# Performance work log

Measured on AMD Instinct MI355X. Metric: run time of the kernel, lower is better.

## Reference

```python
import jax, jax.numpy as jnp
import numpy as np

B = 1024
N_CPGS = 20000
N_FREQS = N_CPGS // 2 + 1  # 10001
HIDDEN = (256, 128, 64)
LN_EPS = 1e-5


def setup_inputs() -> dict:
    key = jax.random.key(0)
    keys = jax.random.split(key, 16)
    inp = {"x": jax.random.normal(keys[0], (B, N_CPGS), dtype=jnp.float32)}
    in_dim = N_FREQS
    for i, h in enumerate(HIDDEN):
        inp[f"W{i}"] = jax.random.normal(keys[1 + i], (h, in_dim), dtype=jnp.float32) * 0.01
        inp[f"alpha{i}"] = jnp.full((h, in_dim), 0.01, dtype=jnp.float32)
        inp[f"b{i}"] = jnp.zeros((h,), dtype=jnp.float32)
        inp[f"eta{i}"] = jnp.asarray(0.1, dtype=jnp.float32)
        inp[f"g{i}"] = jnp.ones((h,), dtype=jnp.float32)   # LayerNorm gamma
        inp[f"be{i}"] = jnp.zeros((h,), dtype=jnp.float32)  # LayerNorm beta
        in_dim = h
    inp["head_w"] = jax.random.normal(keys[10], (1, in_dim), dtype=jnp.float32) * (1.0 / np.sqrt(in_dim))
    inp["head_b"] = jnp.zeros((1,), dtype=jnp.float32)
    return inp


def _hebbian_layer(x, W, alpha, b, eta):
    # y_slow = x W^T + b;  plastic[b,i] = eta * tanh(y_slow)[b,i] * sum_j sigmoid(alpha)[i,j] * x_norm[b,j] * x[b,j]
    y_slow = jnp.einsum('bd,hd->bh', x, W) + b
    x_norm = x / (jnp.linalg.norm(x, axis=-1, keepdims=True) + 1e-8)
    c = x_norm * x  # (B, in) -- collapses the (B,out,in) outer-product trace algebraically
    plastic = eta * jnp.tanh(y_slow) * jnp.einsum('bd,hd->bh', c, jax.nn.sigmoid(alpha))
    return y_slow + plastic


def _layer_norm(h, g, be):
    mu = jnp.mean(h, axis=-1, keepdims=True)
    var = jnp.mean((h - mu) ** 2, axis=-1, keepdims=True)
    return (h - mu) * jax.lax.rsqrt(var + LN_EPS) * g + be


def reference(x, W0, alpha0, b0, eta0, g0, be0,
              W1, alpha1, b1, eta1, g1, be1,
              W2, alpha2, b2, eta2, g2, be2,
              head_w, head_b):
    # FFT spectral front-end
    xc = x - jnp.mean(x, axis=1, keepdims=True)
    h = jnp.log1p(jnp.abs(jnp.fft.rfft(xc, axis=1)))  # (B, N_FREQS)
    params = [(W0, alpha0, b0, eta0, g0, be0),
              (W1, alpha1, b1, eta1, g1, be1),
              (W2, alpha2, b2, eta2, g2, be2)]
    for (W, a, b, eta, g, be) in params:
        h = jax.nn.gelu(_layer_norm(_hebbian_layer(h, W, a, b, eta), g, be), approximate=False)
        # dropout is identity in eval mode
    return (jnp.einsum('bd,od->bo', h, head_w) + head_b)[:, 0]  # (B,)
```

## Files before the change

kernel.cpp:

```cpp
#include <hip/hip_runtime.h>
#include <hip/hip_bf16.h>
#include <math.h>

typedef short bf16x8 __attribute__((ext_vector_type(8)));
typedef float f32x4 __attribute__((ext_vector_type(4)));

static __device__ __forceinline__ unsigned short f2bf(float f) {
    unsigned int u = __float_as_uint(f);
    unsigned int r = (u + 0x7fffu + ((u >> 16) & 1u)) >> 16;
    return (unsigned short)r;
}

static __device__ __forceinline__ bf16x8 sq_bf16x8(bf16x8 a) {
    bf16x8 r;
    #pragma unroll
    for (int i = 0; i < 8; ++i) {
        unsigned int u = ((unsigned int)(unsigned short)a[i]) << 16;
        float f = __uint_as_float(u);
        f *= f;
        r[i] = (short)f2bf(f);
    }
    return r;
}

static __device__ __forceinline__ float gelu_f(float x) {
    return 0.5f * x * (1.f + erff(x * 0.70710678118654752f));
}

static __device__ __forceinline__ void gload_lds16(const void* g, void* l) {
    __builtin_amdgcn_global_load_lds(
        (const __attribute__((address_space(1))) unsigned int*)g,
        (__attribute__((address_space(3))) unsigned int*)l, 16, 0, 0);
}

static __device__ __forceinline__ int ldsmap(int i) { return i + (i >> 6); }

static __device__ __forceinline__ int rev4(int k) {
    int d0 = k % 10; k /= 10;
    int d1 = k % 10; k /= 10;
    int d2 = k % 10; int d3 = k / 10;
    return d0 * 1000 + d1 * 100 + d2 * 10 + d3;
}

__global__ __launch_bounds__(256)
void init_tables_kernel(unsigned int* __restrict__ idxTab)
{
    int i = blockIdx.x * 256 + threadIdx.x;
    if (i < 10001) {
        int k1 = (i == 10000) ? 0 : i;
        int k2 = (k1 == 0) ? 0 : 10000 - k1;
        unsigned a = (unsigned)ldsmap(rev4(k1));
        unsigned b = (unsigned)ldsmap(rev4(k2));
        idxTab[i] = a | (b << 16);
    }
}

static __device__ __forceinline__ void dft5(
    float a0r, float a0i, float a1r, float a1i, float a2r, float a2i,
    float a3r, float a3i, float a4r, float a4i,
    float* Xr, float* Xi)
{
    const float c1 = 0.30901699437494742f, c2 = -0.80901699437494745f;
    const float s1 = 0.95105651629515357f, s2 = 0.58778525229247312f;
    float t1r = a1r + a4r, t1i = a1i + a4i;
    float d1r = a1r - a4r, d1i = a1i - a4i;
    float t2r = a2r + a3r, t2i = a2i + a3i;
    float d2r = a2r - a3r, d2i = a2i - a3i;
    Xr[0] = a0r + t1r + t2r; Xi[0] = a0i + t1i + t2i;
    float m1r = a0r + c1 * t1r + c2 * t2r, m1i = a0i + c1 * t1i + c2 * t2i;
    float m2r = a0r + c2 * t1r + c1 * t2r, m2i = a0i + c2 * t1i + c1 * t2i;
    float n1r = s1 * d1r + s2 * d2r, n1i = s1 * d1i + s2 * d2i;
    float n2r = s2 * d1r - s1 * d2r, n2i = s2 * d1i - s1 * d2i;
    Xr[1] = m1r + n1i; Xi[1] = m1i - n1r;
    Xr[4] = m1r - n1i; Xi[4] = m1i + n1r;
    Xr[2] = m2r + n2i; Xi[2] = m2i - n2r;
    Xr[3] = m2r - n2i; Xi[3] = m2i + n2r;
}

template<int S>
static __device__ __forceinline__ void radix10_core(
    float* __restrict__ reb, float* __restrict__ imb,
    const float* ar, const float* ai, int base, int j)
{
    constexpr int L  = (S == 0) ? 1000 : (S == 1) ? 100 : (S == 2) ? 10 : 1;
    constexpr int SC = (S == 0) ? 1 : (S == 1) ? 10 : (S == 2) ? 100 : 1000;
    constexpr bool TW = (S != 3);

    const float WR[5] = {1.f, 0.80901699437494745f, 0.30901699437494742f,
                         -0.30901699437494742f, -0.80901699437494745f};
    const float WI[5] = {0.f, -0.58778525229247312f, -0.95105651629515357f,
                         -0.95105651629515357f, -0.58778525229247312f};

    float Er[5], Ei[5], Or[5], Oi[5];
    dft5(ar[0], ai[0], ar[2], ai[2], ar[4], ai[4], ar[6], ai[6], ar[8], ai[8], Er, Ei);
    dft5(ar[1], ai[1], ar[3], ai[3], ar[5], ai[5], ar[7], ai[7], ar[9], ai[9], Or, Oi);
    #pragma unroll
    for (int k = 1; k < 5; ++k) {
        float tr = Or[k] * WR[k] - Oi[k] * WI[k];
        Oi[k] = Or[k] * WI[k] + Oi[k] * WR[k];
        Or[k] = tr;
    }

    if (TW) {
        const float ang = (float)(j * SC) * -6.28318530717958648e-4f;
        float w1c, w1s;
        __sincosf(ang, &w1s, &w1c);
        float twr[10], twi[10];
        twr[0] = 1.f; twi[0] = 0.f;
        #pragma unroll
        for (int t = 1; t < 10; ++t) {
            twr[t] = twr[t - 1] * w1c - twi[t - 1] * w1s;
            twi[t] = twr[t - 1] * w1s + twi[t - 1] * w1c;
        }
        #pragma unroll
        for (int k = 0; k < 5; ++k) {
            float xr0 = Er[k] + Or[k], xi0 = Ei[k] + Oi[k];
            float xr1 = Er[k] - Or[k], xi1 = Ei[k] - Oi[k];
            int i0 = ldsmap(base + k * L);
            int i1 = ldsmap(base + (k + 5) * L);
            if (k == 0) {
                reb[i0] = xr0;
                imb[i0] = xi0;
            } else {
                reb[i0] = xr0 * twr[k] - xi0 * twi[k];
                imb[i0] = xr0 * twi[k] + xi0 * twr[k];
            }
            reb[i1] = xr1 * twr[k + 5] - xi1 * twi[k + 5];
            imb[i1] = xr1 * twi[k + 5] + xi1 * twr[k + 5];
        }
    } else {
        #pragma unroll
        for (int k = 0; k < 5; ++k) {
            int i0 = ldsmap(base + k * L);
            int i1 = ldsmap(base + (k + 5) * L);
            reb[i0] = Er[k] + Or[k]; imb[i0] = Ei[k] + Oi[k];
            reb[i1] = Er[k] - Or[k]; imb[i1] = Ei[k] - Oi[k];
        }
    }
}

template<int S>
static __device__ __forceinline__ void radix10_stage(
    float* __restrict__ reb, float* __restrict__ imb, int tid)
{
    constexpr int L = (S == 1) ? 100 : (S == 2) ? 10 : 1;
    for (int w = tid; w < 1000; w += 512) {
        int g, j;
        if (S == 3) { g = w; j = 0; }
        else        { g = w / L; j = w - g * L; }
        const int base = g * (10 * L) + j;
        float ar[10], ai[10];
        #pragma unroll
        for (int u = 0; u < 10; ++u) {
            int idx = ldsmap(base + u * L);
            ar[u] = reb[idx];
            ai[u] = imb[idx];
        }
        radix10_core<S>(reb, imb, ar, ai, base, j);
    }
}

__global__ __launch_bounds__(512, 4)
void fft_prep_kernel(const float* __restrict__ x,
                     unsigned short* __restrict__ hb,
                     float* __restrict__ hnorm,
                     const float* __restrict__ W0, const float* __restrict__ A0,
                     unsigned short* __restrict__ Wb, unsigned short* __restrict__ Sb,
                     const float* __restrict__ W1, const float* __restrict__ A1,
                     const float* __restrict__ W2, const float* __restrict__ A2,
                     float* __restrict__ W1T, float* __restrict__ S1T,
                     float* __restrict__ W2T, float* __restrict__ S2T,
                     const unsigned int* __restrict__ idxTab)
{
    if (blockIdx.x >= 1024) {
        int idx = (blockIdx.x - 1024) * 512 + threadIdx.x;
        if (idx < 1280128) {
            const bool isW = idx < 640064;
            const int f4 = isW ? idx : idx - 640064;
            const float* src = isW ? W0 : A0;
            unsigned short* dst = isW ? Wb : Sb;
            float4 v = ((const float4*)src)[f4];
            float e[4] = {v.x, v.y, v.z, v.w};
            int flat = f4 * 4;
            int row = flat / 10001;
            int col = flat - row * 10001;
            #pragma unroll
            for (int i = 0; i < 4; ++i) {
                if (col == 10001) { row++; col = 0; }
                float val = isW ? e[i] : 1.f / (1.f + expf(-e[i]));
                dst[(size_t)row * 10240 + col] = f2bf(val);
                col++;
            }
        } else if (idx < 1341312) {
            int i = idx - 1280128;
            int row = i / 239;
            int col = 10001 + (i - row * 239);
            Wb[(size_t)row * 10240 + col] = 0;
            Sb[(size_t)row * 10240 + col] = 0;
        } else if (idx < 1423232) {
            int o = idx - 1341312;
            if (o < 32768) {
                int d = o >> 7, h = o & 127;
                W1T[o] = W1[h * 256 + d];
            } else if (o < 65536) {
                int p = o - 32768;
                int d = p >> 7, h = p & 127;
                S1T[p] = 1.f / (1.f + expf(-A1[h * 256 + d]));
            } else if (o < 73728) {
                int p = o - 65536;
                int d = p >> 6, h = p & 63;
                W2T[p] = W2[h * 128 + d];
            } else {
                int p = o - 73728;
                int d = p >> 6, h = p & 63;
                S2T[p] = 1.f / (1.f + expf(-A2[h * 128 + d]));
            }
        }
        return;
    }

    __shared__ float reb[10156];
    __shared__ float imb[10156];
    __shared__ float redbuf[8];

    const int b = blockIdx.x;
    const int tid = threadIdx.x;
    const int lane = tid & 63;
    const int wv = tid >> 6;

    const float2* z2 = (const float2*)(x + (size_t)b * 20000);
    for (int w = tid; w < 1000; w += 512) {
        float ar[10], ai[10];
        #pragma unroll
        for (int u = 0; u < 10; ++u) {
            float2 v = z2[w + u * 1000];
            ar[u] = v.x; ai[u] = v.y;
        }
        radix10_core<0>(reb, imb, ar, ai, w, w);
    }
    __syncthreads();
    radix10_stage<1>(reb, imb, tid);
    __syncthreads();
    radix10_stage<2>(reb, imb, tid);
    __syncthreads();
    radix10_stage<3>(reb, imb, tid);
    __syncthreads();

    float ct, st;
    __sincosf((float)tid * -3.14159265358979324e-4f, &st, &ct);
    const float RC = 0.987091579f;
    const float RS = -0.160156842f;
    float sumsq = 0.f;
    unsigned short* hrow = hb + (size_t)b * 10240;
    #pragma unroll
    for (int i = 0; i < 20; ++i) {
        int k = tid + i * 512;
        float hval = 0.f;
        if (k > 0 && k <= 10000) {
            unsigned pp = idxTab[k];
            int i1 = (int)(pp & 0xffffu);
            int i2 = (int)(pp >> 16);
            float zr = reb[i1], zi = imb[i1];
            float wr = reb[i2], wi = imb[i2];
            float er = 0.5f * (zr + wr);
            float ei = 0.5f * (zi - wi);
            float odr = 0.5f * (zi + wi);
            float odi = -0.5f * (zr - wr);
            float xre = er + ct * odr - st * odi;
            float xim = ei + ct * odi + st * odr;
            hval = __logf(1.f + sqrtf(xre * xre + xim * xim));
        }
        hrow[k] = f2bf(hval);
        sumsq += hval * hval;
        float nct = ct * RC - st * RS;
        st = ct * RS + st * RC;
        ct = nct;
    }
    #pragma unroll
    for (int o = 32; o; o >>= 1) sumsq += __shfl_xor(sumsq, o);
    __syncthreads();
    if (lane == 0) redbuf[wv] = sumsq;
    __syncthreads();
    if (tid == 0) {
        float tsq = 0.f;
        #pragma unroll
        for (int i = 0; i < 8; ++i) tsq += redbuf[i];
        hnorm[b] = 1.f / (sqrtf(tsq) + 1e-8f);
    }
}

__global__ __launch_bounds__(256, 3)
void gemm0_kernel(const unsigned short* __restrict__ hb,
                  const unsigned short* __restrict__ Wb, const unsigned short* __restrict__ Sb,
                  float* __restrict__ Py, float* __restrict__ Pp)
{
    __shared__ unsigned short Ah[128 * 64];
    __shared__ unsigned short Bw[64 * 64];
    __shared__ unsigned short Bs[64 * 64];

    const int t = threadIdx.x;
    const int lin = blockIdx.x;
    const int xcd = lin & 7;
    const int sub = lin >> 3;
    const int z = xcd * 2 + (sub & 1);
    const int tile = sub >> 1;
    const int b0 = (tile & 7) * 128;
    const int n0 = (tile >> 3) * 64;

    const int lane = t & 63;
    const int wv = t >> 6;
    const int ml = lane & 15;
    const int q4 = lane >> 4;
    const int s0 = q4 ^ (ml & 7);

    const int sub8 = lane >> 3;
    const int sl = lane & 7;
    const int gsw = sl ^ sub8;

    f32x4 accY[2][4], accP[2][4];
    #pragma unroll
    for (int mt = 0; mt < 2; ++mt)
        #pragma unroll
        for (int nt = 0; nt < 4; ++nt) {
            accY[mt][nt] = (f32x4){0.f, 0.f, 0.f, 0.f};
            accP[mt][nt] = (f32x4){0.f, 0.f, 0.f, 0.f};
        }

    const int kbase = z * 640;

    for (int step = 0; step < 10; ++step) {
        const int k0 = kbase + step * 64;
        __syncthreads();
        #pragma unroll
        for (int j = 0; j < 4; ++j) {
            const int c = wv * 4 + j;
            const size_t go = (size_t)(b0 + c * 8 + sub8) * 10240 + k0 + gsw * 8;
            gload_lds16(&hb[go], &Ah[c * 512]);
        }
        #pragma unroll
        for (int j = 0; j < 2; ++j) {
            const int c = wv * 2 + j;
            const size_t go = (size_t)(n0 + c * 8 + sub8) * 10240 + k0 + gsw * 8;
            gload_lds16(&Wb[go], &Bw[c * 512]);
            gload_lds16(&Sb[go], &Bs[c * 512]);
        }
        __syncthreads();

        #pragma unroll
        for (int kk = 0; kk < 2; ++kk) {
            const int slot = (s0 ^ (kk << 2)) << 3;
            bf16x8 ah[2], ac[2], bw[4], bs[4];
            #pragma unroll
            for (int mt = 0; mt < 2; ++mt) {
                int mrow = wv * 32 + mt * 16 + ml;
                ah[mt] = *(const bf16x8*)&Ah[mrow * 64 + slot];
                ac[mt] = sq_bf16x8(ah[mt]);
            }
            #pragma unroll
            for (int nt = 0; nt < 4; ++nt) {
                int nrow = nt * 16 + ml;
                bw[nt] = *(const bf16x8*)&Bw[nrow * 64 + slot];
                bs[nt] = *(const bf16x8*)&Bs[nrow * 64 + slot];
            }
            #pragma unroll
            for (int mt = 0; mt < 2; ++mt)
                #pragma unroll
                for (int nt = 0; nt < 4; ++nt) {
                    accY[mt][nt] = __builtin_amdgcn_mfma_f32_16x16x32_bf16(ah[mt], bw[nt], accY[mt][nt], 0, 0, 0);
                    accP[mt][nt] = __builtin_amdgcn_mfma_f32_16x16x32_bf16(ac[mt], bs[nt], accP[mt][nt], 0, 0, 0);
                }
        }
    }

    const int rq = q4 * 4;
    #pragma unroll
    for (int mt = 0; mt < 2; ++mt)
        #pragma unroll
        for (int nt = 0; nt < 4; ++nt)
            #pragma unroll
            for (int r = 0; r < 4; ++r) {
                int m = b0 + wv * 32 + mt * 16 + rq + r;
                int n = n0 + nt * 16 + ml;
                size_t o = ((size_t)z * 1024 + m) * 256 + n;
                Py[o] = accY[mt][nt][r];
                Pp[o] = accP[mt][nt][r];
            }
}

__global__ __launch_bounds__(256)
void combine_tail_kernel(const float* __restrict__ Py, const float* __restrict__ Pp,
                 const float* __restrict__ hnorm,
                 const float* __restrict__ b0v, const float* __restrict__ eta0p,
                 const float* __restrict__ g0, const float* __restrict__ be0,
                 const float* __restrict__ W1T, const float* __restrict__ S1T,
                 const float* __restrict__ b1, const float* __restrict__ eta1p,
                 const float* __restrict__ g1, const float* __restrict__ be1,
                 const float* __restrict__ W2T, const float* __restrict__ S2T,
                 const float* __restrict__ b2, const float* __restrict__ eta2p,
                 const float* __restrict__ g2, const float* __restrict__ be2,
                 const float* __restrict__ hw, const float* __restrict__ hbod,
                 float* __restrict__ out)
{
    __shared__ float sh[2][256];
    __shared__ float sc[2][256];
    __shared__ float sv[2][128];
    __shared__ float sh2[2][128];
    __shared__ float sc2[2][128];
    __shared__ float sv2[2][64];
    __shared__ float p2a[2][2][64];
    __shared__ float p2b[2][2][64];
    __shared__ float redA[4][2];
    __shared__ float redB[4][2];

    const int t = threadIdx.x;
    const int b0 = blockIdx.x * 2;
    const int lane = t & 63;
    const int wv = t >> 6;

    const float e0 = eta0p[0];
    const float bias0 = b0v[t];
    float ys[2] = {0.f, 0.f}, ps[2] = {0.f, 0.f};
    #pragma unroll 4
    for (int s = 0; s < 16; ++s)
        #pragma unroll
        for (int r = 0; r < 2; ++r) {
            size_t o = ((size_t)s * 1024 + b0 + r) * 256 + t;
            ys[r] += Py[o];
            ps[r] += Pp[o];
        }
    float v[2];
    #pragma unroll
    for (int r = 0; r < 2; ++r) {
        float p = ps[r] * hnorm[b0 + r];
        float y = ys[r] + bias0;
        v[r] = y + e0 * tanhf(y) * p;
    }

    float s1[2], s2[2];
    #pragma unroll
    for (int r = 0; r < 2; ++r) { s1[r] = v[r]; s2[r] = v[r] * v[r]; }
    #pragma unroll
    for (int o = 32; o; o >>= 1)
        #pragma unroll
        for (int r = 0; r < 2; ++r) { s1[r] += __shfl_xor(s1[r], o); s2[r] += __shfl_xor(s2[r], o); }
    if (lane == 0)
        #pragma unroll
        for (int r = 0; r < 2; ++r) { redA[wv][r] = s1[r]; redB[wv][r] = s2[r]; }
    __syncthreads();

    const float gg = g0[t], bb = be0[t];
    float gl[2], s3[2];
    #pragma unroll
    for (int r = 0; r < 2; ++r) {
        float sum = redA[0][r] + redA[1][r] + redA[2][r] + redA[3][r];
        float sumsq = redB[0][r] + redB[1][r] + redB[2][r] + redB[3][r];
        float mu = sum * (1.f / 256.f);
        float var = sumsq * (1.f / 256.f) - mu * mu;
        float u = (v[r] - mu) * rsqrtf(var + 1e-5f) * gg + bb;
        gl[r] = gelu_f(u);
        s3[r] = gl[r] * gl[r];
    }
    #pragma unroll
    for (int o = 32; o; o >>= 1)
        #pragma unroll
        for (int r = 0; r < 2; ++r) s3[r] += __shfl_xor(s3[r], o);
    __syncthreads();
    if (lane == 0)
        #pragma unroll
        for (int r = 0; r < 2; ++r) redA[wv][r] = s3[r];
    __syncthreads();
    #pragma unroll
    for (int r = 0; r < 2; ++r) {
        float gsq = redA[0][r] + redA[1][r] + redA[2][r] + redA[3][r];
        float inv = 1.f / (sqrtf(gsq) + 1e-8f);
        sh[r][t] = gl[r];
        sc[r][t] = gl[r] * gl[r] * inv;
    }
    __syncthreads();

    const int hcol = t & 127;
    const int r1 = t >> 7;
    float ya = 0.f, pa = 0.f;
    #pragma unroll 8
    for (int d = 0; d < 256; ++d) {
        ya += sh[r1][d] * W1T[d * 128 + hcol];
        pa += sc[r1][d] * S1T[d * 128 + hcol];
    }
    {
        const float e1 = eta1p[0];
        float y = ya + b1[hcol];
        sv[r1][hcol] = y + e1 * tanhf(y) * pa;
    }
    __syncthreads();

    if (wv < 2) {
        int r = wv;
        float v0 = sv[r][lane];
        float v1 = sv[r][lane + 64];
        float s = v0 + v1, sq = v0 * v0 + v1 * v1;
        #pragma unroll
        for (int o = 32; o; o >>= 1) { s += __shfl_xor(s, o); sq += __shfl_xor(sq, o); }
        float mu = s * (1.f / 128.f);
        float var = sq * (1.f / 128.f) - mu * mu;
        float rs = rsqrtf(var + 1e-5f);
        float u0 = (v0 - mu) * rs * g1[lane] + be1[lane];
        float u1 = (v1 - mu) * rs * g1[lane + 64] + be1[lane + 64];
        float ge0 = gelu_f(u0);
        float ge1 = gelu_f(u1);
        float gsq = ge0 * ge0 + ge1 * ge1;
        #pragma unroll
        for (int o = 32; o; o >>= 1) gsq += __shfl_xor(gsq, o);
        float inv = 1.f / (sqrtf(gsq) + 1e-8f);
        sh2[r][lane] = ge0; sh2[r][lane + 64] = ge1;
        sc2[r][lane] = ge0 * ge0 * inv; sc2[r][lane + 64] = ge1 * ge1 * inv;
    }
    __syncthreads();

    {
        const int h2c = t & 63;
        const int r = (t >> 6) & 1;
        const int dh = t >> 7;
        float yb = 0.f, pb = 0.f;
        #pragma unroll 8
        for (int dd = 0; dd < 64; ++dd) {
            int d = dh * 64 + dd;
            yb += sh2[r][d] * W2T[d * 64 + h2c];
            pb += sc2[r][d] * S2T[d * 64 + h2c];
        }
        p2a[dh][r][h2c] = yb;
        p2b[dh][r][h2c] = pb;
    }
    __syncthreads();
    if (t < 128) {
        const int h2c = t & 63;
        const int r = t >> 6;
        const float e2 = eta2p[0];
        float yb = p2a[0][r][h2c] + p2a[1][r][h2c];
        float pb = p2b[0][r][h2c] + p2b[1][r][h2c];
        float y = yb + b2[h2c];
        sv2[r][h2c] = y + e2 * tanhf(y) * pb;
    }
    __syncthreads();

    if (wv < 2) {
        int r = wv;
        float v0 = sv2[r][lane];
        float s = v0, sq = v0 * v0;
        #pragma unroll
        for (int o = 32; o; o >>= 1) { s += __shfl_xor(s, o); sq += __shfl_xor(sq, o); }
        float mu = s * (1.f / 64.f);
        float var = sq * (1.f / 64.f) - mu * mu;
        float rs = rsqrtf(var + 1e-5f);
        float u = (v0 - mu) * rs * g2[lane] + be2[lane];
        float g = gelu_f(u);
        float hc = g * hw[lane];
        #pragma unroll
        for (int o = 32; o; o >>= 1) hc += __shfl_xor(hc, o);
        if (lane == 0) out[b0 + r] = hc + hbod[0];
    }
}

extern "C" void kernel_launch(void* const* d_in, const int* in_sizes, int n_in,
                              void* d_out, int out_size, void* d_ws, size_t ws_size,
                              hipStream_t stream)
{
    const float* x    = (const float*)d_in[0];
    const float* W0   = (const float*)d_in[1];
    const float* A0   = (const float*)d_in[2];
    const float* b0   = (const float*)d_in[3];
    const float* eta0 = (const float*)d_in[4];
    const float* g0   = (const float*)d_in[5];
    const float* be0  = (const float*)d_in[6];
    const float* W1   = (const float*)d_in[7];
    const float* A1   = (const float*)d_in[8];
    const float* b1   = (const float*)d_in[9];
    const float* eta1 = (const float*)d_in[10];
    const float* g1   = (const float*)d_in[11];
    const float* be1  = (const float*)d_in[12];
    const float* W2   = (const float*)d_in[13];
    const float* A2   = (const float*)d_in[14];
    const float* b2   = (const float*)d_in[15];
    const float* eta2 = (const float*)d_in[16];
    const float* g2   = (const float*)d_in[17];
    const float* be2  = (const float*)d_in[18];
    const float* hw   = (const float*)d_in[19];
    const float* hbod = (const float*)d_in[20];
    float* out = (float*)d_out;

    char* w = (char*)d_ws;
    unsigned short* hb  = (unsigned short*)(w + 0);
    unsigned short* Wb0 = (unsigned short*)(w + 20971520);
    unsigned short* Sb0 = (unsigned short*)(w + 26214400);
    float* Py   = (float*)(w + 31457280);
    float* Pp   = (float*)(w + 48234496);
    float* W1T  = (float*)(w + 65011712);
    float* S1T  = (float*)(w + 65142784);
    float* W2T  = (float*)(w + 65273856);
    float* S2T  = (float*)(w + 65306624);
    float* hnm  = (float*)(w + 65339392);
    unsigned int* idxT = (unsigned int*)(w + 65343488);

    hipLaunchKernelGGL(init_tables_kernel, dim3(40), dim3(256), 0, stream, idxT);
    hipLaunchKernelGGL(fft_prep_kernel, dim3(3804), dim3(512), 0, stream,
                       x, hb, hnm, W0, A0, Wb0, Sb0, W1, A1, W2, A2, W1T, S1T, W2T, S2T,
                       idxT);
    hipLaunchKernelGGL(gemm0_kernel, dim3(512), dim3(256), 0, stream, hb, Wb0, Sb0, Py, Pp);
    hipLaunchKernelGGL(combine_tail_kernel, dim3(512), dim3(256), 0, stream, Py, Pp, hnm,
                       b0, eta0, g0, be0, W1T, S1T, b1, eta1, g1, be1,
                       W2T, S2T, b2, eta2, g2, be2, hw, hbod, out);
}
```

Baseline: 251.9 us.

## Split per-row FFT into two four-step passes with fp16 intermediate

The single-block-per-row radix-10^4 FFT is replaced by a four-step 100x100 decomposition. The first kernel does the column FFTs over half a row per block and applies twiddles from precomputed tables, storing the intermediate as half2 in global memory. A second kernel does the row FFTs, the real-FFT unpacking and log1p-magnitude, and accumulates the row norm with atomics. This doubles the number of blocks per row and shrinks LDS per block to raise occupancy, at the cost of an extra global round trip, an extra launch and fp16 precision loss in the intermediate.

```diff
diff --git a/kernel.cpp b/kernel.cpp
--- a/kernel.cpp
+++ b/kernel.cpp
@@ -1,5 +1,6 @@
 #include <hip/hip_runtime.h>
 #include <hip/hip_bf16.h>
+#include <hip/hip_fp16.h>
 #include <math.h>
 
 typedef short bf16x8 __attribute__((ext_vector_type(8)));
@@ -33,26 +34,24 @@
         (__attribute__((address_space(3))) unsigned int*)l, 16, 0, 0);
 }
 
-static __device__ __forceinline__ int ldsmap(int i) { return i + (i >> 6); }
-
-static __device__ __forceinline__ int rev4(int k) {
-    int d0 = k % 10; k /= 10;
-    int d1 = k % 10; k /= 10;
-    int d2 = k % 10; int d3 = k / 10;
-    return d0 * 1000 + d1 * 100 + d2 * 10 + d3;
-}
+static __device__ __forceinline__ int rev2(int k) { return (k % 10) * 10 + k / 10; }
 
 __global__ __launch_bounds__(256)
-void init_tables_kernel(unsigned int* __restrict__ idxTab)
+void init_tables_kernel(float2* __restrict__ T2, float2* __restrict__ twF1,
+                        float* __restrict__ hacc)
 {
     int i = blockIdx.x * 256 + threadIdx.x;
-    if (i < 10001) {
-        int k1 = (i == 10000) ? 0 : i;
-        int k2 = (k1 == 0) ? 0 : 10000 - k1;
-        unsigned a = (unsigned)ldsmap(rev4(k1));
-        unsigned b = (unsigned)ldsmap(rev4(k2));
-        idxTab[i] = a | (b << 16);
-    }
+    if (i < 90) {
+        int t = i / 10 + 1, j = i % 10;
+        double ang = (double)(100 * j * t) * -6.2831853071795864769e-4;
+        T2[i] = make_float2((float)cos(ang), (float)sin(ang));
+    }
+    if (i < 10000) {
+        int k2 = i / 100, n1 = i % 100;
+        double ang = (double)(n1 * k2) * -6.2831853071795864769e-4;
+        twF1[i] = make_float2((float)cos(ang), (float)sin(ang));
+    }
+    if (i < 1024) hacc[i] = 0.f;
 }
 
 static __device__ __forceinline__ void dft5(
@@ -77,20 +76,21 @@
     Xr[3] = m2r - n2i; Xi[3] = m2i + n2r;
 }
 
-template<int S>
-static __device__ __forceinline__ void radix10_core(
+template<bool DOTW>
+static __device__ __forceinline__ void r10f(
     float* __restrict__ reb, float* __restrict__ imb,
-    const float* ar, const float* ai, int base, int j)
-{
-    constexpr int L  = (S == 0) ? 1000 : (S == 1) ? 100 : (S == 2) ? 10 : 1;
-    constexpr int SC = (S == 0) ? 1 : (S == 1) ? 10 : (S == 2) ? 100 : 1000;
-    constexpr bool TW = (S != 3);
-
+    int base, int stride, int j, const float2* __restrict__ tw)
+{
     const float WR[5] = {1.f, 0.80901699437494745f, 0.30901699437494742f,
                          -0.30901699437494742f, -0.80901699437494745f};
     const float WI[5] = {0.f, -0.58778525229247312f, -0.95105651629515357f,
                          -0.95105651629515357f, -0.58778525229247312f};
-
+    float ar[10], ai[10];
+    #pragma unroll
+    for (int u = 0; u < 10; ++u) {
+        ar[u] = reb[base + u * stride];
+        ai[u] = imb[base + u * stride];
+    }
     float Er[5], Ei[5], Or[5], Oi[5];
     dft5(ar[0], ai[0], ar[2], ai[2], ar[4], ai[4], ar[6], ai[6], ar[8], ai[8], Er, Ei);
     dft5(ar[1], ai[1], ar[3], ai[3], ar[5], ai[5], ar[7], ai[7], ar[9], ai[9], Or, Oi);
@@ -100,28 +100,21 @@
         Oi[k] = Or[k] * WI[k] + Oi[k] * WR[k];
         Or[k] = tr;
     }
-
-    if (TW) {
-        const float ang = (float)(j * SC) * -6.28318530717958648e-4f;
-        float w1c, w1s;
-        __sincosf(ang, &w1s, &w1c);
+    if (DOTW) {
         float twr[10], twi[10];
-        twr[0] = 1.f; twi[0] = 0.f;
         #pragma unroll
         for (int t = 1; t < 10; ++t) {
-            twr[t] = twr[t - 1] * w1c - twi[t - 1] * w1s;
-            twi[t] = twr[t - 1] * w1s + twi[t - 1] * w1c;
+            float2 w_ = tw[(t - 1) * 10 + j];
+            twr[t] = w_.x; twi[t] = w_.y;
         }
         #pragma unroll
         for (int k = 0; k < 5; ++k) {
             float xr0 = Er[k] + Or[k], xi0 = Ei[k] + Oi[k];
             float xr1 = Er[k] - Or[k], xi1 = Ei[k] - Oi[k];
-            int i0 = ldsmap(base + k * L);
-            int i1 = ldsmap(base + (k + 5) * L);
-            if (k == 0) {
-                reb[i0] = xr0;
-                imb[i0] = xi0;
-            } else {
+            int i0 = base + k * stride;
+            int i1 = base + (k + 5) * stride;
+            if (k == 0) { reb[i0] = xr0; imb[i0] = xi0; }
+            else {
                 reb[i0] = xr0 * twr[k] - xi0 * twi[k];
                 imb[i0] = xr0 * twi[k] + xi0 * twr[k];
             }
@@ -131,49 +124,26 @@
     } else {
         #pragma unroll
         for (int k = 0; k < 5; ++k) {
-            int i0 = ldsmap(base + k * L);
-            int i1 = ldsmap(base + (k + 5) * L);
+            int i0 = base + k * stride;
+            int i1 = base + (k + 5) * stride;
             reb[i0] = Er[k] + Or[k]; imb[i0] = Ei[k] + Oi[k];
             reb[i1] = Er[k] - Or[k]; imb[i1] = Ei[k] - Oi[k];
         }
     }
 }
 
-template<int S>
-static __device__ __forceinline__ void radix10_stage(
-    float* __restrict__ reb, float* __restrict__ imb, int tid)
-{
-    constexpr int L = (S == 1) ? 100 : (S == 2) ? 10 : 1;
-    for (int w = tid; w < 1000; w += 512) {
-        int g, j;
-        if (S == 3) { g = w; j = 0; }
-        else        { g = w / L; j = w - g * L; }
-        const int base = g * (10 * L) + j;
-        float ar[10], ai[10];
-        #pragma unroll
-        for (int u = 0; u < 10; ++u) {
-            int idx = ldsmap(base + u * L);
-            ar[u] = reb[idx];
-            ai[u] = imb[idx];
-        }
-        radix10_core<S>(reb, imb, ar, ai, base, j);
-    }
-}
-
-__global__ __launch_bounds__(512, 4)
-void fft_prep_kernel(const float* __restrict__ x,
-                     unsigned short* __restrict__ hb,
-                     float* __restrict__ hnorm,
-                     const float* __restrict__ W0, const float* __restrict__ A0,
-                     unsigned short* __restrict__ Wb, unsigned short* __restrict__ Sb,
-                     const float* __restrict__ W1, const float* __restrict__ A1,
-                     const float* __restrict__ W2, const float* __restrict__ A2,
-                     float* __restrict__ W1T, float* __restrict__ S1T,
-                     float* __restrict__ W2T, float* __restrict__ S2T,
-                     const unsigned int* __restrict__ idxTab)
-{
-    if (blockIdx.x >= 1024) {
-        int idx = (blockIdx.x - 1024) * 512 + threadIdx.x;
+__global__ __launch_bounds__(512)
+void fft1_prep_kernel(const float* __restrict__ x, __half2* __restrict__ G2,
+                      const float* __restrict__ W0, const float* __restrict__ A0,
+                      unsigned short* __restrict__ Wb, unsigned short* __restrict__ Sb,
+                      const float* __restrict__ W1, const float* __restrict__ A1,
+                      const float* __restrict__ W2, const float* __restrict__ A2,
+                      float* __restrict__ W1T, float* __restrict__ S1T,
+                      float* __restrict__ W2T, float* __restrict__ S2T,
+                      const float2* __restrict__ T2, const float2* __restrict__ twF1)
+{
+    if (blockIdx.x >= 2048) {
+        int idx = (blockIdx.x - 2048) * 512 + threadIdx.x;
         if (idx < 1280128) {
             const bool isW = idx < 640064;
             const int f4 = isW ? idx : idx - 640064;
@@ -219,73 +189,135 @@
         return;
     }
 
-    __shared__ float reb[10156];
-    __shared__ float imb[10156];
+    __shared__ float reb[50 * 101];
+    __shared__ float imb[50 * 101];
+
+    const int t = threadIdx.x;
+    const int rb = blockIdx.x >> 1;
+    const int c0 = (blockIdx.x & 1) * 50;
+
+    const float2* z2 = (const float2*)(x + (size_t)rb * 20000);
+    for (int f = t; f < 5000; f += 512) {
+        int n2 = f / 50, dn1 = f - n2 * 50;
+        float2 v = z2[n2 * 100 + c0 + dn1];
+        reb[dn1 * 101 + n2] = v.x;
+        imb[dn1 * 101 + n2] = v.y;
+    }
+    __syncthreads();
+    if (t < 500) {
+        int c = t / 10, j = t - c * 10;
+        r10f<true>(reb, imb, c * 101 + j, 10, j, T2);
+    }
+    __syncthreads();
+    if (t < 500) {
+        int c = t / 10, g = t - c * 10;
+        r10f<false>(reb, imb, c * 101 + g * 10, 1, 0, (const float2*)nullptr);
+    }
+    __syncthreads();
+    __half2* Grow = G2 + (size_t)rb * 10000;
+    for (int f = t; f < 5000; f += 512) {
+        int p = f / 50, dn1 = f - p * 50;
+        int n1 = c0 + dn1;
+        int k2 = rev2(p);
+        float vr = reb[dn1 * 101 + p];
+        float vi = imb[dn1 * 101 + p];
+        float2 w_ = twF1[k2 * 100 + n1];
+        float gr = vr * w_.x - vi * w_.y;
+        float gi = vr * w_.y + vi * w_.x;
+        Grow[k2 * 100 + n1] = __floats2half2_rn(gr, gi);
+    }
+}
+
+__global__ __launch_bounds__(512)
+void fft2_kernel(const __half2* __restrict__ G2,
+                 unsigned short* __restrict__ hb,
+                 float* __restrict__ hacc,
+                 const float2* __restrict__ T2)
+{
+    __shared__ float reb[51 * 101];
+    __shared__ float imb[51 * 101];
     __shared__ float redbuf[8];
 
-    const int b = blockIdx.x;
-    const int tid = threadIdx.x;
-    const int lane = tid & 63;
-    const int wv = tid >> 6;
-
-    const float2* z2 = (const float2*)(x + (size_t)b * 20000);
-    for (int w = tid; w < 1000; w += 512) {
-        float ar[10], ai[10];
-        #pragma unroll
-        for (int u = 0; u < 10; ++u) {
-            float2 v = z2[w + u * 1000];
-            ar[u] = v.x; ai[u] = v.y;
-        }
-        radix10_core<0>(reb, imb, ar, ai, w, w);
-    }
-    __syncthreads();
-    radix10_stage<1>(reb, imb, tid);
-    __syncthreads();
-    radix10_stage<2>(reb, imb, tid);
-    __syncthreads();
-    radix10_stage<3>(reb, imb, tid);
-    __syncthreads();
-
-    float ct, st;
-    __sincosf((float)tid * -3.14159265358979324e-4f, &st, &ct);
-    const float RC = 0.987091579f;
-    const float RS = -0.160156842f;
-    float sumsq = 0.f;
-    unsigned short* hrow = hb + (size_t)b * 10240;
-    #pragma unroll
-    for (int i = 0; i < 20; ++i) {
-        int k = tid + i * 512;
-        float hval = 0.f;
-        if (k > 0 && k <= 10000) {
-            unsigned pp = idxTab[k];
-            int i1 = (int)(pp & 0xffffu);
-            int i2 = (int)(pp >> 16);
-            float zr = reb[i1], zi = imb[i1];
-            float wr = reb[i2], wi = imb[i2];
-            float er = 0.5f * (zr + wr);
-            float ei = 0.5f * (zi - wi);
-            float odr = 0.5f * (zi + wi);
-            float odi = -0.5f * (zr - wr);
-            float xre = er + ct * odr - st * odi;
-            float xim = ei + ct * odi + st * odr;
-            hval = __logf(1.f + sqrtf(xre * xre + xim * xim));
-        }
-        hrow[k] = f2bf(hval);
-        sumsq += hval * hval;
-        float nct = ct * RC - st * RS;
-        st = ct * RS + st * RC;
-        ct = nct;
-    }
-    #pragma unroll
-    for (int o = 32; o; o >>= 1) sumsq += __shfl_xor(sumsq, o);
-    __syncthreads();
-    if (lane == 0) redbuf[wv] = sumsq;
-    __syncthreads();
-    if (tid == 0) {
+    const int t = threadIdx.x;
+    const int rb = blockIdx.x >> 1;
+    const int half = blockIdx.x & 1;
+    const int NC = half ? 49 : 51;
+
+    const __half2* Grow = G2 + (size_t)rb * 10000;
+    for (int f = t; f < NC * 100; f += 512) {
+        int s = f / 100, n1 = f - s * 100;
+        int k2 = half ? (26 + s) : (s <= 25 ? s : s + 49);
+        float2 v = __half22float2(Grow[k2 * 100 + n1]);
+        reb[s * 101 + n1] = v.x;
+        imb[s * 101 + n1] = v.y;
+    }
+    __syncthreads();
+    if (t < NC * 10) {
+        int s = t / 10, j = t - s * 10;
+        r10f<true>(reb, imb, s * 101 + j, 10, j, T2);
+    }
+    __syncthreads();
+    if (t < NC * 10) {
+        int s = t / 10, g = t - s * 10;
+        r10f<false>(reb, imb, s * 101 + g * 10, 1, 0, (const float2*)nullptr);
+    }
+    __syncthreads();
+
+    unsigned short* hrow = hb + (size_t)rb * 10240;
+    float lsum = 0.f;
+    {
+        int s = t >> 3, o = t & 7;
+        if (s < NC) {
+            int k2 = half ? (26 + s) : (s <= 25 ? s : s + 49);
+            int ps = half ? (48 - s) : (s == 0 ? 0 : 51 - s);
+            int k1a = o * 13;
+            int k1b = k1a + 13 < 100 ? k1a + 13 : 100;
+            float ct, st;
+            __sincosf((float)(100 * k1a + k2) * -3.14159265358979324e-4f, &st, &ct);
+            const float RC = 0.99950656036573160f;
+            const float RS = -0.031410759078128293f;
+            for (int k1 = k1a; k1 < k1b; ++k1) {
+                int k = 100 * k1 + k2;
+                if (k == 0) {
+                    float xn = reb[0] - imb[0];
+                    float hval = __logf(1.f + fabsf(xn));
+                    hrow[10000] = f2bf(hval);
+                    lsum += hval * hval;
+                } else {
+                    int i1 = s * 101 + rev2(k1);
+                    int k1p = (k2 == 0) ? (100 - k1) : (99 - k1);
+                    int i2 = ps * 101 + rev2(k1p);
+                    float zr = reb[i1], zi = imb[i1];
+                    float wr = reb[i2], wi = imb[i2];
+                    float er = 0.5f * (zr + wr);
+                    float ei = 0.5f * (zi - wi);
+                    float odr = 0.5f * (zi + wi);
+                    float odi = -0.5f * (zr - wr);
+                    float xre = er + ct * odr - st * odi;
+                    float xim = ei + ct * odi + st * odr;
+                    float hval = __logf(1.f + sqrtf(xre * xre + xim * xim));
+                    hrow[k] = f2bf(hval);
+                    lsum += hval * hval;
+                }
+                float nct = ct * RC - st * RS;
+                st = ct * RS + st * RC;
+                ct = nct;
+            }
+        }
+    }
+    if (half == 0) {
+        if (t < 239) hrow[10001 + t] = 0;
+        if (t == 239) hrow[0] = 0;
+    }
+    #pragma unroll
+    for (int o = 32; o; o >>= 1) lsum += __shfl_xor(lsum, o);
+    if ((t & 63) == 0) redbuf[t >> 6] = lsum;
+    __syncthreads();
+    if (t == 0) {
         float tsq = 0.f;
         #pragma unroll
         for (int i = 0; i < 8; ++i) tsq += redbuf[i];
-        hnorm[b] = 1.f / (sqrtf(tsq) + 1e-8f);
+        atomicAdd(&hacc[rb], tsq);
     }
 }
 
@@ -389,7 +421,7 @@
 
 __global__ __launch_bounds__(256)
 void combine_tail_kernel(const float* __restrict__ Py, const float* __restrict__ Pp,
-                 const float* __restrict__ hnorm,
+                 const float* __restrict__ hacc,
                  const float* __restrict__ b0v, const float* __restrict__ eta0p,
                  const float* __restrict__ g0, const float* __restrict__ be0,
                  const float* __restrict__ W1T, const float* __restrict__ S1T,
@@ -431,7 +463,8 @@
     float v[2];
     #pragma unroll
     for (int r = 0; r < 2; ++r) {
-        float p = ps[r] * hnorm[b0 + r];
+        float hn = 1.f / (sqrtf(hacc[b0 + r]) + 1e-8f);
+        float p = ps[r] * hn;
         float y = ys[r] + bias0;
         v[r] = y + e0 * tanhf(y) * p;
     }
@@ -591,21 +624,24 @@
     unsigned short* hb  = (unsigned short*)(w + 0);
     unsigned short* Wb0 = (unsigned short*)(w + 20971520);
     unsigned short* Sb0 = (unsigned short*)(w + 26214400);
+    __half2* G2 = (__half2*)(w + 31457280);
     float* Py   = (float*)(w + 31457280);
     float* Pp   = (float*)(w + 48234496);
-    float* W1T  = (float*)(w + 65011712);
-    float* S1T  = (float*)(w + 65142784);
-    float* W2T  = (float*)(w + 65273856);
-    float* S2T  = (float*)(w + 65306624);
-    float* hnm  = (float*)(w + 65339392);
-    unsigned int* idxT = (unsigned int*)(w + 65343488);
-
-    hipLaunchKernelGGL(init_tables_kernel, dim3(40), dim3(256), 0, stream, idxT);
-    hipLaunchKernelGGL(fft_prep_kernel, dim3(3804), dim3(512), 0, stream,
-                       x, hb, hnm, W0, A0, Wb0, Sb0, W1, A1, W2, A2, W1T, S1T, W2T, S2T,
-                       idxT);
+    float* W1T  = (float*)(w + 72417280);
+    float* S1T  = (float*)(w + 72548352);
+    float* W2T  = (float*)(w + 72679424);
+    float* S2T  = (float*)(w + 72712192);
+    float* hacc = (float*)(w + 72744960);
+    float2* T2  = (float2*)(w + 72749056);
+    float2* twF1= (float2*)(w + 72749824);
+
+    hipLaunchKernelGGL(init_tables_kernel, dim3(40), dim3(256), 0, stream, T2, twF1, hacc);
+    hipLaunchKernelGGL(fft1_prep_kernel, dim3(4828), dim3(512), 0, stream,
+                       x, G2, W0, A0, Wb0, Sb0, W1, A1, W2, A2, W1T, S1T, W2T, S2T,
+                       T2, twF1);
+    hipLaunchKernelGGL(fft2_kernel, dim3(2048), dim3(512), 0, stream, G2, hb, hacc, T2);
     hipLaunchKernelGGL(gemm0_kernel, dim3(512), dim3(256), 0, stream, hb, Wb0, Sb0, Py, Pp);
-    hipLaunchKernelGGL(combine_tail_kernel, dim3(512), dim3(256), 0, stream, Py, Pp, hnm,
+    hipLaunchKernelGGL(combine_tail_kernel, dim3(512), dim3(256), 0, stream, Py, Pp, hacc,
                        b0, eta0, g0, be0, W1T, S1T, b1, eta1, g1, be1,
                        W2T, S2T, b2, eta2, g2, be2, hw, hbod, out);
 }
```

Measured after the change: 293.0 us. +16.3%, slower.
